# Kernel optimization log

Measured on AMD Instinct MI355X. Metric: run time of the kernel, lower is better.

The kernel has to match this reference:

```python
import jax, jax.numpy as jnp
import numpy as np

SIGMA = 32.0        # Gaussian prior bandwidth (init sigma)
ADJ_RATIO = 0.2     # fraction of neighbors kept per row in feature adjacency
NEG_SLOPE = 0.01    # LeakyReLU slope
EPS = 1e-8


def setup_inputs() -> dict:
    key = jax.random.key(0)
    k0, k1, k2, k3 = jax.random.split(key, 4)
    N, D, L = 8192, 128, 2
    x = jax.random.normal(k0, (N, D), dtype=jnp.float32)
    importances = jax.random.uniform(k1, (N, 1), dtype=jnp.float32)
    W1 = jax.random.normal(k2, (L, D, D), dtype=jnp.float32) / np.float32(np.sqrt(D))
    W2 = jax.random.normal(k3, (L, D, D), dtype=jnp.float32) / np.float32(np.sqrt(D))
    return {"x": x, "importances": importances, "W1": W1, "W2": W2, "batch_size": N}


def _build_adj_prior(imp, eye):
    # Gaussian kernel on pairwise importance differences: [N,N]
    d = imp - imp.T
    A = jnp.exp(-(d * d) / SIGMA) + eye  # self loop
    return A / jnp.sum(A, axis=1, keepdims=True)  # row-normalize


def _build_adj_feature(x, eye, k):
    # cosine similarity, keep top adj_ratio*N entries per row, self loop, row-normalize
    xn = x / (jnp.linalg.norm(x, axis=1, keepdims=True) + EPS)
    S = xn @ xn.T  # [N,N]
    thr = jax.lax.top_k(S, k)[0][:, -1:]  # per-row k-th largest value
    A = jnp.where(S >= thr, S, jnp.zeros_like(S)) + eye
    return A / jnp.sum(A, axis=1, keepdims=True)


def reference(x, importances, W1, W2, batch_size):
    N = batch_size
    k = int(ADJ_RATIO * N)
    eye = jnp.eye(N, dtype=x.dtype)
    L = W1.shape[0]
    h = x
    for l in range(L):  # fixed small layer count
        h = x  # clone before layer (used in final residual)
        adj_prior = _build_adj_prior(importances, eye)
        adj_feat = _build_adj_feature(x, eye, k)
        # graph conv over both adjacencies: A @ (x @ W)
        x = jax.nn.leaky_relu(adj_prior @ (x @ W1[l]) + adj_feat @ (x @ W2[l]),
                              negative_slope=NEG_SLOPE)
    return x + h * importances
```

## Files before the change

kernel.cpp:

```cpp
#include <hip/hip_runtime.h>
#include <hip/hip_bf16.h>

typedef __bf16 bf16x8 __attribute__((ext_vector_type(8)));
typedef float f32x4 __attribute__((ext_vector_type(4)));
typedef unsigned short u16x2 __attribute__((ext_vector_type(2)));
typedef short s16x2 __attribute__((ext_vector_type(2)));
typedef unsigned u32x4 __attribute__((ext_vector_type(4)));
typedef __hip_bfloat16 bf16;

static constexpr int NN = 8192;
static constexpr int DD = 128;
static constexpr int KTOP = 1638;
static constexpr int KSLICE = 8;
static constexpr int KCH = NN / KSLICE;

__device__ __forceinline__ void gll16(const void* g, void* l) {
  __builtin_amdgcn_global_load_lds((const __attribute__((address_space(1))) void*)g,
                                   (__attribute__((address_space(3))) void*)l, 16, 0, 0);
}

__global__ void detect_dtype(const unsigned short* __restrict__ xin, int* __restrict__ flag) {
  __shared__ int cnt;
  if (threadIdx.x == 0) cnt = 0;
  __syncthreads();
  int c = 0;
  for (int i = threadIdx.x; i < 4096; i += 256) {
    int e = (xin[i] >> 7) & 0xFF;
    if (e >= 0x8A) ++c;
  }
  atomicAdd(&cnt, c);
  __syncthreads();
  if (threadIdx.x == 0) *flag = (cnt > 16) ? 1 : 0;
}

__global__ void prep(const void* __restrict__ imp_in,
                     const void* __restrict__ W1, const void* __restrict__ W2,
                     float* __restrict__ impf,
                     bf16* __restrict__ Wt1, bf16* __restrict__ Wt2,
                     const int* __restrict__ flag) {
  int isf32 = *flag;
  int b = blockIdx.x;
  if (b == 0) {
    for (int i = threadIdx.x; i < NN; i += 256)
      impf[i] = isf32 ? ((const float*)imp_in)[i] : __bfloat162float(((const bf16*)imp_in)[i]);
  } else {
    int w = b - 1;
    const void* srcv = (w < 2 ? W1 : W2);
    bf16* dst = (w < 2 ? Wt1 : Wt2) + (w & 1) * DD * DD;
    int off = (w & 1) * DD * DD;
    for (int f = threadIdx.x; f < DD * DD; f += 256) {
      int n = f >> 7, k = f & 127;
      float v = isf32 ? ((const float*)srcv)[off + k * DD + n]
                      : __bfloat162float(((const bf16*)srcv)[off + k * DD + n]);
      dst[n * DD + k] = __float2bfloat16(v);
    }
  }
}

__global__ void rownorm(const void* __restrict__ src, const int* __restrict__ flag, int raw,
                        bf16* __restrict__ xnb, bf16* __restrict__ xb) {
  int wave = threadIdx.x >> 6;
  int lane = threadIdx.x & 63;
  int row = blockIdx.x * 4 + wave;
  float vx, vy;
  if (raw && *flag == 0) {
    unsigned u = ((const unsigned*)src)[(long)row * 64 + lane];
    vx = __uint_as_float(u << 16);
    vy = __uint_as_float(u & 0xFFFF0000u);
  } else {
    float2 v = ((const float2*)src)[(long)row * 64 + lane];
    vx = v.x; vy = v.y;
  }
  float s = vx * vx + vy * vy;
  for (int off = 1; off < 64; off <<= 1) s += __shfl_xor(s, off);
  float inv = 1.0f / (sqrtf(s) + 1e-8f);
  int c = lane * 2;
  xb[(long)row * DD + c]      = __float2bfloat16(vx);
  xb[(long)row * DD + c + 1]  = __float2bfloat16(vy);
  xnb[(long)row * DD + c]     = __float2bfloat16(vx * inv);
  xnb[(long)row * DD + c + 1] = __float2bfloat16(vy * inv);
}

__launch_bounds__(256)
__global__ void prior_reduce(const float* __restrict__ impf, const bf16* __restrict__ Yt1,
                             float* __restrict__ Mt, float* __restrict__ Gt) {
  __shared__ float red[5][4];
  int c = blockIdx.x;
  int tid = threadIdx.x;
  float s[5] = {0.f, 0.f, 0.f, 0.f, 0.f};
  bool hasY = (c < 128);
  const bf16* col = Yt1 + (long)(hasY ? c : 0) * NN;
  for (int j = tid; j < NN; j += 256) {
    float d = impf[j];
    float a = __expf(d * d * (-1.0f / 32.0f));
    float p = hasY ? a * __bfloat162float(col[j]) : a;
    #pragma unroll
    for (int t = 0; t < 5; ++t) { s[t] += p; p *= d; }
  }
  #pragma unroll
  for (int t = 0; t < 5; ++t)
    for (int off = 1; off < 64; off <<= 1) s[t] += __shfl_xor(s[t], off);
  int wave = tid >> 6, lane = tid & 63;
  if (lane == 0)
    #pragma unroll
    for (int t = 0; t < 5; ++t) red[t][wave] = s[t];
  __syncthreads();
  if (tid == 0) {
    #pragma unroll
    for (int t = 0; t < 5; ++t) {
      float v = red[t][0] + red[t][1] + red[t][2] + red[t][3];
      if (hasY) Mt[t * 128 + c] = v; else Gt[t] = v;
    }
  }
}

__device__ __forceinline__ void gemm_core(const bf16* __restrict__ A, const bf16* __restrict__ Bt,
                                          long rowA0, long rowB0, int tid,
                                          bf16* __restrict__ Yt,
                                          bf16* __restrict__ RM, long rm_ld) {
  __shared__ bf16 lA[128][136];
  __shared__ bf16 lB[64][136];
  for (int i = 0; i < 8; ++i) {
    int f = tid + i * 256;
    int r = f >> 4, kg = f & 15;
    *reinterpret_cast<uint4*>(&lA[r][kg * 8]) =
        *reinterpret_cast<const uint4*>(A + (rowA0 + r) * DD + kg * 8);
  }
  for (int i = 0; i < 4; ++i) {
    int f = tid + i * 256;
    int r = f >> 4, kg = f & 15;
    *reinterpret_cast<uint4*>(&lB[r][kg * 8]) =
        *reinterpret_cast<const uint4*>(Bt + (rowB0 + r) * DD + kg * 8);
  }
  __syncthreads();
  int wave = tid >> 6, lane = tid & 63;
  int wm = (wave >> 1) * 64;
  int wn = (wave & 1) * 32;
  int quad = lane >> 4, l16 = lane & 15;
  f32x4 acc[4][2];
  #pragma unroll
  for (int mi = 0; mi < 4; ++mi)
    #pragma unroll
    for (int ni = 0; ni < 2; ++ni) acc[mi][ni] = {0.f, 0.f, 0.f, 0.f};
  #pragma unroll
  for (int ks = 0; ks < 4; ++ks) {
    int kb = ks * 32 + quad * 8;
    bf16x8 af[4], bfr[2];
    #pragma unroll
    for (int mi = 0; mi < 4; ++mi)
      af[mi] = *reinterpret_cast<const bf16x8*>(&lA[wm + mi * 16 + l16][kb]);
    #pragma unroll
    for (int ni = 0; ni < 2; ++ni)
      bfr[ni] = *reinterpret_cast<const bf16x8*>(&lB[wn + ni * 16 + l16][kb]);
    #pragma unroll
    for (int mi = 0; mi < 4; ++mi)
      #pragma unroll
      for (int ni = 0; ni < 2; ++ni)
        acc[mi][ni] = __builtin_amdgcn_mfma_f32_16x16x32_bf16(af[mi], bfr[ni], acc[mi][ni], 0, 0, 0);
  }
  if (Yt) {
    #pragma unroll
    for (int mi = 0; mi < 4; ++mi)
      #pragma unroll
      for (int ni = 0; ni < 2; ++ni) {
        long rowb = rowA0 + wm + mi * 16 + quad * 4;
        long col = rowB0 + wn + ni * 16 + l16;
        bf16 t4[4];
        #pragma unroll
        for (int r = 0; r < 4; ++r) t4[r] = __float2bfloat16(acc[mi][ni][r]);
        *reinterpret_cast<ushort4*>(Yt + col * (long)NN + rowb) =
            *reinterpret_cast<const ushort4*>(t4);
      }
  }
  __syncthreads();
  bf16 (*cs)[72] = reinterpret_cast<bf16(*)[72]>(&lA[0][0]);
  #pragma unroll
  for (int mi = 0; mi < 4; ++mi)
    #pragma unroll
    for (int ni = 0; ni < 2; ++ni)
      #pragma unroll
      for (int r = 0; r < 4; ++r)
        cs[wm + mi * 16 + quad * 4 + r][wn + ni * 16 + l16] = __float2bfloat16(acc[mi][ni][r]);
  __syncthreads();
  #pragma unroll
  for (int i = 0; i < 4; ++i) {
    int f = tid + i * 256;
    int r = f >> 3, sg = f & 7;
    *reinterpret_cast<uint4*>(RM + (rowA0 + r) * rm_ld + rowB0 + sg * 8) =
        *reinterpret_cast<const uint4*>(&cs[r][sg * 8]);
  }
}

__launch_bounds__(256)
__global__ void gemm_s_sym(const bf16* __restrict__ Xn, bf16* __restrict__ S) {
  int bi = blockIdx.y, bj = blockIdx.x;
  if (bj < bi) return;
  __shared__ bf16 lA[128][136];
  __shared__ bf16 lB[128][136];
  int tid = threadIdx.x;
  long rowA0 = (long)bi * 128, rowB0 = (long)bj * 128;
  for (int i = 0; i < 8; ++i) {
    int f = tid + i * 256;
    int r = f >> 4, kg = f & 15;
    *reinterpret_cast<uint4*>(&lA[r][kg * 8]) =
        *reinterpret_cast<const uint4*>(Xn + (rowA0 + r) * DD + kg * 8);
    *reinterpret_cast<uint4*>(&lB[r][kg * 8]) =
        *reinterpret_cast<const uint4*>(Xn + (rowB0 + r) * DD + kg * 8);
  }
  __syncthreads();
  int wave = tid >> 6, lane = tid & 63;
  int wm = (wave >> 1) * 64;
  int wn = (wave & 1) * 64;
  int quad = lane >> 4, l16 = lane & 15;
  f32x4 acc[4][4];
  #pragma unroll
  for (int mi = 0; mi < 4; ++mi)
    #pragma unroll
    for (int ni = 0; ni < 4; ++ni) acc[mi][ni] = {0.f, 0.f, 0.f, 0.f};
  #pragma unroll
  for (int ks = 0; ks < 4; ++ks) {
    int kb = ks * 32 + quad * 8;
    bf16x8 af[4], bfr[4];
    #pragma unroll
    for (int mi = 0; mi < 4; ++mi)
      af[mi] = *reinterpret_cast<const bf16x8*>(&lA[wm + mi * 16 + l16][kb]);
    #pragma unroll
    for (int ni = 0; ni < 4; ++ni)
      bfr[ni] = *reinterpret_cast<const bf16x8*>(&lB[wn + ni * 16 + l16][kb]);
    #pragma unroll
    for (int mi = 0; mi < 4; ++mi)
      #pragma unroll
      for (int ni = 0; ni < 4; ++ni)
        acc[mi][ni] = __builtin_amdgcn_mfma_f32_16x16x32_bf16(af[mi], bfr[ni], acc[mi][ni], 0, 0, 0);
  }
  ushort4 q4[4][4];
  #pragma unroll
  for (int mi = 0; mi < 4; ++mi)
    #pragma unroll
    for (int ni = 0; ni < 4; ++ni) {
      unsigned short t4[4];
      #pragma unroll
      for (int r = 0; r < 4; ++r) {
        float vv = acc[mi][ni][r];
        vv = vv > 0.f ? vv : 0.f;
        bf16 b = __float2bfloat16(vv);
        t4[r] = *reinterpret_cast<unsigned short*>(&b);
      }
      q4[mi][ni] = *reinterpret_cast<const ushort4*>(t4);
    }
  __syncthreads();
  bf16 (*cs)[136]  = reinterpret_cast<bf16(*)[136]>(&lA[0][0]);
  bf16 (*csT)[136] = reinterpret_cast<bf16(*)[136]>(&lB[0][0]);
  #pragma unroll
  for (int mi = 0; mi < 4; ++mi)
    #pragma unroll
    for (int ni = 0; ni < 4; ++ni) {
      int row = wm + mi * 16 + quad * 4;
      int col = wn + ni * 16 + l16;
      const unsigned short* t4 = reinterpret_cast<const unsigned short*>(&q4[mi][ni]);
      #pragma unroll
      for (int r = 0; r < 4; ++r)
        *reinterpret_cast<unsigned short*>(&cs[row + r][col]) = t4[r];
      *reinterpret_cast<ushort4*>(&csT[col][row]) = q4[mi][ni];
    }
  __syncthreads();
  #pragma unroll
  for (int i = 0; i < 8; ++i) {
    int f = tid + i * 256;
    int r = f >> 4, sg = f & 15;
    *reinterpret_cast<uint4*>(S + (rowA0 + r) * NN + rowB0 + sg * 8) =
        *reinterpret_cast<const uint4*>(&cs[r][sg * 8]);
  }
  if (bi != bj) {
    #pragma unroll
    for (int i = 0; i < 8; ++i) {
      int f = tid + i * 256;
      int r = f >> 4, sg = f & 15;
      *reinterpret_cast<uint4*>(S + (rowB0 + r) * NN + rowA0 + sg * 8) =
          *reinterpret_cast<const uint4*>(&csT[r][sg * 8]);
    }
  }
}

__launch_bounds__(256)
__global__ void gemm_y_dual(const bf16* __restrict__ xb,
                            const bf16* __restrict__ Wt1, const bf16* __restrict__ Wt2,
                            bf16* __restrict__ Yt1, bf16* __restrict__ Yt2,
                            bf16* __restrict__ Yr1, bf16* __restrict__ Yr2) {
  int sel = blockIdx.x >> 1;
  int bx = blockIdx.x & 1;
  gemm_core(xb, sel ? Wt2 : Wt1, (long)blockIdx.y * 128, (long)bx * 64, threadIdx.x,
            sel ? Yt2 : Yt1, sel ? Yr2 : Yr1, DD);
}

__launch_bounds__(256)
__global__ void topk_thresh(const bf16* __restrict__ S, unsigned short* __restrict__ kthr,
                            float* __restrict__ invRsF) {
  __shared__ unsigned hist[4][1088];
  int wave = threadIdx.x >> 6, lane = threadIdx.x & 63;
  long row = (long)blockIdx.x * 4 + wave;
  unsigned* h = hist[wave];
  #pragma unroll
  for (int j = 0; j < 17; ++j) h[lane + j * 64] = 0;
  __syncthreads();

  const uint4* rp = reinterpret_cast<const uint4*>(S + row * NN) + lane;
  unsigned hs = 0;
  #pragma unroll
  for (int t = 0; t < 16; ++t) {
    uint4 v = rp[t * 64];
    unsigned a4[4] = {v.x, v.y, v.z, v.w};
    #pragma unroll
    for (int e = 0; e < 4; ++e) {
      unsigned u = a4[e];
      hs |= u;
      s16x2 d = __builtin_bit_cast(s16x2, u) - __builtin_bit_cast(s16x2, 0x3BFF3BFFu);
      d = __builtin_elementwise_max(d, (s16x2)0);
      d = __builtin_elementwise_min(d, (s16x2)1024);
      unsigned bins = __builtin_bit_cast(unsigned, d);
      unsigned blo = bins & 0xFFFFu, bhi = bins >> 16;
      if (blo) atomicAdd(&h[blo], 1u);
      if (bhi) atomicAdd(&h[bhi], 1u);
    }
  }
  __syncthreads();

  unsigned c[17], sfx[17];
  #pragma unroll
  for (int j = 0; j < 17; ++j) c[j] = h[lane * 17 + j];
  unsigned run = 0;
  #pragma unroll
  for (int j = 16; j >= 0; --j) { run += c[j]; sfx[j] = run; }
  unsigned incl = sfx[0];
  #pragma unroll
  for (int off = 1; off < 64; off <<= 1) {
    unsigned t = __shfl_down(incl, off);
    incl += (lane + off < 64) ? t : 0u;
  }
  unsigned above = incl - sfx[0];
  int cand = -1;
  #pragma unroll
  for (int j = 16; j >= 0; --j) {
    int b = lane * 17 + j;
    if (cand < 0 && b >= 1 && above + sfx[j] >= (unsigned)KTOP) cand = b;
  }
  int best = cand;
  #pragma unroll
  for (int off = 1; off < 64; off <<= 1) {
    int t = __shfl_xor(best, off);
    best = t > best ? t : best;
  }
  int thrbin = best >= 1 ? best : 1;
  unsigned thr = 0x3BFFu + (unsigned)thrbin;

  float fs = 0.f;
  #pragma unroll
  for (int j = 0; j < 17; ++j) {
    int b = lane * 17 + j;
    float val = __uint_as_float((0x3BFFu + (unsigned)b) << 16);
    fs += (b >= thrbin) ? (float)c[j] * val : 0.f;
  }
  if (__ballot(hs & 0x40004000u)) {
    float v1024 = __uint_as_float(0x3FFF0000u);
    #pragma unroll 1
    for (int t = 0; t < 16; ++t) {
      uint4 v = rp[t * 64];
      unsigned a4[4] = {v.x, v.y, v.z, v.w};
      for (int e = 0; e < 4; ++e) {
        unsigned lo = a4[e] & 0xFFFFu, hi = a4[e] >> 16;
        if (lo >= 0x4000u && lo < 0x8000u) fs += __uint_as_float(lo << 16) - v1024;
        if (hi >= 0x4000u && hi < 0x8000u) fs += __uint_as_float(hi << 16) - v1024;
      }
    }
  }
  #pragma unroll
  for (int off = 1; off < 64; off <<= 1) fs += __shfl_xor(fs, off);
  if (lane == 0) {
    invRsF[row] = 1.0f / (fs + 1.0f);
    kthr[row] = (unsigned short)thr;
  }
}

__launch_bounds__(256)
__global__ void fused_av_partial(const bf16* __restrict__ S, const bf16* __restrict__ Yt2,
                                 const unsigned short* __restrict__ kthr,
                                 float* __restrict__ Pacc) {
  __shared__ bf16 lS[2][128][64];
  __shared__ bf16 lY[2][128][64];
  int tid = threadIdx.x;
  int wave = tid >> 6, lane = tid & 63;
  long row0 = (long)blockIdx.x * 128;
  long kbase = (long)blockIdx.y * KCH;
  int quad = lane >> 4, l16 = lane & 15;
  int wm = (wave >> 1) * 64;
  int wn = (wave & 1) * 64;
  int swz = (l16 & 7) << 4;

  int sj = lane >> 3, sseg = lane & 7;
  long swb = (long)((sseg ^ sj) << 4);
  const char* gS[4];
  const char* gY[4];
  #pragma unroll
  for (int j = 0; j < 4; ++j) {
    long srow = row0 + (long)(wave * 4 + j) * 8 + sj;
    gS[j] = (const char*)S + (srow * NN + kbase) * 2 + swb;
    long ycol = (long)(wave * 4 + j) * 8 + sj;
    gY[j] = (const char*)Yt2 + (ycol * (long)NN + kbase) * 2 + swb;
  }
  unsigned pp[4];
  #pragma unroll
  for (int mi = 0; mi < 4; ++mi) {
    unsigned p = kthr[row0 + wm + mi * 16 + l16];
    pp[mi] = (p << 16) | p;
  }
  f32x4 acc[4][4];
  #pragma unroll
  for (int mi = 0; mi < 4; ++mi)
    #pragma unroll
    for (int ni = 0; ni < 4; ++ni) acc[mi][ni] = {0.f, 0.f, 0.f, 0.f};

  constexpr int NT = KCH / 64;
  {
    char* lsb = (char*)&lS[0][0][0];
    char* lyb = (char*)&lY[0][0][0];
    #pragma unroll
    for (int j = 0; j < 4; ++j) { gll16(gS[j], lsb + (wave * 4 + j) * 1024); gS[j] += 128; }
    #pragma unroll
    for (int j = 0; j < 4; ++j) { gll16(gY[j], lyb + (wave * 4 + j) * 1024); gY[j] += 128; }
  }
  #pragma unroll 1
  for (int t = 0; t < NT; ++t) {
    int cur = t & 1;
    if (t + 1 < NT) {
      char* lsb = (char*)&lS[cur ^ 1][0][0];
      char* lyb = (char*)&lY[cur ^ 1][0][0];
      #pragma unroll
      for (int j = 0; j < 4; ++j) { gll16(gS[j], lsb + (wave * 4 + j) * 1024); gS[j] += 128; }
      #pragma unroll
      for (int j = 0; j < 4; ++j) { gll16(gY[j], lyb + (wave * 4 + j) * 1024); gY[j] += 128; }
      asm volatile("s_waitcnt vmcnt(8)" ::: "memory");
    } else {
      asm volatile("s_waitcnt vmcnt(0)" ::: "memory");
    }
    __builtin_amdgcn_s_barrier();
    const char* lsb = (const char*)&lS[cur][0][0];
    const char* lyb = (const char*)&lY[cur][0][0];
    #pragma unroll
    for (int ks = 0; ks < 2; ++ks) {
      int cb = ks * 64 + quad * 16;
      int cbs = cb ^ swz;
      bf16x8 av[4], bv[4];
      #pragma unroll
      for (int mi = 0; mi < 4; ++mi) {
        int r = wm + mi * 16 + l16;
        u32x4 uu = *reinterpret_cast<const u32x4*>(lsb + r * 128 + cbs);
        #pragma unroll
        for (int e = 0; e < 4; ++e) {
          unsigned tb = uu[e] | 0x80008000u;
          u16x2 d = __builtin_bit_cast(u16x2, tb) - __builtin_bit_cast(u16x2, pp[mi]);
          s16x2 msk = __builtin_bit_cast(s16x2, d) >> 15;
          uu[e] &= __builtin_bit_cast(unsigned, msk);
        }
        av[mi] = __builtin_bit_cast(bf16x8, uu);
      }
      #pragma unroll
      for (int ni = 0; ni < 4; ++ni) {
        int c = wn + ni * 16 + l16;
        bv[ni] = *reinterpret_cast<const bf16x8*>(lyb + c * 128 + cbs);
      }
      #pragma unroll
      for (int mi = 0; mi < 4; ++mi)
        #pragma unroll
        for (int ni = 0; ni < 4; ++ni)
          acc[mi][ni] = __builtin_amdgcn_mfma_f32_16x16x32_bf16(av[mi], bv[ni], acc[mi][ni], 0, 0, 0);
    }
    __builtin_amdgcn_s_barrier();
  }
  float* out = Pacc + (long)blockIdx.y * NN * DD;
  #pragma unroll
  for (int mi = 0; mi < 4; ++mi)
    #pragma unroll
    for (int ni = 0; ni < 4; ++ni)
      #pragma unroll
      for (int r = 0; r < 4; ++r) {
        long row = row0 + wm + mi * 16 + quad * 4 + r;
        int col = wn + ni * 16 + l16;
        out[row * DD + col] = acc[mi][ni][r];
      }
}

__global__ void epilogue(const float* __restrict__ Pacc, const bf16* __restrict__ Yr1,
                         const bf16* __restrict__ Yr2, const float* __restrict__ Gt,
                         const float* __restrict__ Mt, const float* __restrict__ invRsF,
                         const float* __restrict__ impf,
                         float* __restrict__ Xout, const float* __restrict__ hres,
                         float* __restrict__ outf) {
  int i = blockIdx.x * 256 + threadIdx.x;
  int row = i >> 7, col = i & 127;
  float acc = 0.f;
  #pragma unroll
  for (int s = 0; s < KSLICE; ++s) acc += Pacc[((long)s * NN + row) * DD + col];
  float d = impf[row];
  float a = __expf(d * d * (-1.0f / 32.0f));
  const float ct[5] = {1.0f, 1.0f / 16.0f, 1.0f / 512.0f, 1.0f / 24576.0f, 1.0f / 1572864.0f};
  float g[5];
  float p = a;
  #pragma unroll
  for (int t = 0; t < 5; ++t) { g[t] = ct[t] * p; p *= d; }
  float rs = 1.0f;
  #pragma unroll
  for (int t = 0; t < 5; ++t) rs += g[t] * Gt[t];
  float inv = 1.0f / rs;
  float pv[5];
  #pragma unroll
  for (int t = 0; t < 5; ++t) pv[t] = g[t] * inv;
  float y1 = __bfloat162float(Yr1[i]);
  float y2 = __bfloat162float(Yr2[i]);
  float prior = inv * y1 + pv[0] * Mt[col] + pv[1] * Mt[128 + col] + pv[2] * Mt[256 + col]
              + pv[3] * Mt[384 + col] + pv[4] * Mt[512 + col];
  float v = prior + invRsF[row] * (acc + y2);
  v = v > 0.f ? v : 0.01f * v;
  if (outf) outf[i] = v + hres[i] * impf[row];
  else      Xout[i] = v;
}


extern "C" void kernel_launch(void* const* d_in, const int* in_sizes, int n_in,
                              void* d_out, int out_size, void* d_ws, size_t ws_size,
                              hipStream_t stream) {
  const void* x_in   = d_in[0];
  const void* imp_in = d_in[1];
  const void* W1 = d_in[2];
  const void* W2 = d_in[3];
  float* out = (float*)d_out;

  char* ws = (char*)d_ws;
  size_t o = 0;
  auto alloc = [&](size_t bytes) { void* p = ws + o; o += (bytes + 511) & ~511ull; return p; };
  bf16*  Af   = (bf16*)alloc((size_t)NN * NN * 2);
  float* Pacc = (float*)alloc((size_t)KSLICE * NN * DD * 4);
  float* xf1  = (float*)alloc((size_t)NN * DD * 4);
  bf16*  xnb  = (bf16*)alloc((size_t)NN * DD * 2);
  bf16*  xb   = (bf16*)alloc((size_t)NN * DD * 2);
  bf16*  Yt1  = (bf16*)alloc((size_t)NN * DD * 2);
  bf16*  Yt2  = (bf16*)alloc((size_t)NN * DD * 2);
  bf16*  Yr1  = (bf16*)alloc((size_t)NN * DD * 2);
  bf16*  Yr2  = (bf16*)alloc((size_t)NN * DD * 2);
  bf16*  Wt1  = (bf16*)alloc((size_t)2 * DD * DD * 2);
  bf16*  Wt2  = (bf16*)alloc((size_t)2 * DD * DD * 2);
  float* impf = (float*)alloc((size_t)NN * 4);
  float* Mt   = (float*)alloc((size_t)5 * 128 * 4);
  float* Gt   = (float*)alloc((size_t)8 * 4);
  float* invRsF = (float*)alloc((size_t)NN * 4);
  unsigned short* kthr = (unsigned short*)alloc((size_t)NN * 2);
  int*   dflag  = (int*)alloc(64);
  (void)ws_size; (void)n_in; (void)in_sizes; (void)out_size;

  detect_dtype<<<1, 256, 0, stream>>>((const unsigned short*)x_in, dflag);
  prep<<<5, 256, 0, stream>>>(imp_in, W1, W2, impf, Wt1, Wt2, dflag);

  for (int l = 0; l < 2; ++l) {
    rownorm<<<NN / 4, 256, 0, stream>>>(l ? (const void*)xf1 : x_in, dflag, l ? 0 : 1, xnb, xb);
    gemm_y_dual<<<dim3(4, 64), 256, 0, stream>>>(xb, Wt1 + l * DD * DD, Wt2 + l * DD * DD,
                                                 Yt1, Yt2, Yr1, Yr2);
    prior_reduce<<<129, 256, 0, stream>>>(impf, Yt1, Mt, Gt);
    gemm_s_sym<<<dim3(64, 64), 256, 0, stream>>>(xnb, Af);
    topk_thresh<<<NN / 4, 256, 0, stream>>>(Af, kthr, invRsF);
    fused_av_partial<<<dim3(NN / 128, KSLICE), 256, 0, stream>>>(Af, Yt2, kthr, Pacc);
    if (l == 0)
      epilogue<<<NN * DD / 256, 256, 0, stream>>>(Pacc, Yr1, Yr2, Gt, Mt, invRsF, impf,
                                                  xf1, nullptr, nullptr);
    else
      epilogue<<<NN * DD / 256, 256, 0, stream>>>(Pacc, Yr1, Yr2, Gt, Mt, invRsF, impf,
                                                  nullptr, xf1, out);
  }
}
```

Before: 354.3 us.

## Fuse split-K reduction and epilogue into AV kernel via last-block counter

Folds dtype detection into the prep kernel, removing one launch. It also moves the split-K reduction and epilogue into fused_av_partial: each of the 8 K-slice blocks for a row tile increments an atomic counter, and the last one to finish sums the partials and applies the prior, leaky ReLU and residual with vectorized loads and stores. This drops two epilogue launches and lets the final reduction run while other tiles are still busy. The cost is a threadfence and atomic per block, and the fused tail runs serially on 64 blocks, so it may load-balance poorly.

```diff
diff --git a/kernel.cpp b/kernel.cpp
--- a/kernel.cpp
+++ b/kernel.cpp
@@ -19,28 +19,26 @@
                                    (__attribute__((address_space(3))) void*)l, 16, 0, 0);
 }
 
-__global__ void detect_dtype(const unsigned short* __restrict__ xin, int* __restrict__ flag) {
-  __shared__ int cnt;
-  if (threadIdx.x == 0) cnt = 0;
+__global__ void prep(const unsigned short* __restrict__ xin, const void* __restrict__ imp_in,
+                     const void* __restrict__ W1, const void* __restrict__ W2,
+                     float* __restrict__ impf,
+                     bf16* __restrict__ Wt1, bf16* __restrict__ Wt2,
+                     int* __restrict__ flag, unsigned* __restrict__ avcnt) {
+  __shared__ int cnt_s;
+  if (threadIdx.x == 0) cnt_s = 0;
   __syncthreads();
   int c = 0;
   for (int i = threadIdx.x; i < 4096; i += 256) {
     int e = (xin[i] >> 7) & 0xFF;
     if (e >= 0x8A) ++c;
   }
-  atomicAdd(&cnt, c);
-  __syncthreads();
-  if (threadIdx.x == 0) *flag = (cnt > 16) ? 1 : 0;
-}
-
-__global__ void prep(const void* __restrict__ imp_in,
-                     const void* __restrict__ W1, const void* __restrict__ W2,
-                     float* __restrict__ impf,
-                     bf16* __restrict__ Wt1, bf16* __restrict__ Wt2,
-                     const int* __restrict__ flag) {
-  int isf32 = *flag;
+  atomicAdd(&cnt_s, c);
+  __syncthreads();
+  int isf32 = (cnt_s > 16) ? 1 : 0;
   int b = blockIdx.x;
   if (b == 0) {
+    if (threadIdx.x == 0) *flag = isf32;
+    if (threadIdx.x < 64) avcnt[threadIdx.x] = 0;
     for (int i = threadIdx.x; i < NN; i += 256)
       impf[i] = isf32 ? ((const float*)imp_in)[i] : __bfloat162float(((const bf16*)imp_in)[i]);
   } else {
@@ -384,7 +382,12 @@
 __launch_bounds__(256)
 __global__ void fused_av_partial(const bf16* __restrict__ S, const bf16* __restrict__ Yt2,
                                  const unsigned short* __restrict__ kthr,
-                                 float* __restrict__ Pacc) {
+                                 float* __restrict__ Pacc, unsigned* __restrict__ avcnt,
+                                 const bf16* __restrict__ Yr1, const bf16* __restrict__ Yr2,
+                                 const float* __restrict__ Gt, const float* __restrict__ Mt,
+                                 const float* __restrict__ invRsF, const float* __restrict__ impf,
+                                 float* __restrict__ Xout, const float* __restrict__ hres,
+                                 float* __restrict__ outf) {
   __shared__ bf16 lS[2][128][64];
   __shared__ bf16 lY[2][128][64];
   int tid = threadIdx.x;
@@ -476,7 +479,7 @@
     }
     __builtin_amdgcn_s_barrier();
   }
-  float* out = Pacc + (long)blockIdx.y * NN * DD;
+  float* pout = Pacc + (long)blockIdx.y * NN * DD;
   #pragma unroll
   for (int mi = 0; mi < 4; ++mi)
     #pragma unroll
@@ -485,43 +488,69 @@
       for (int r = 0; r < 4; ++r) {
         long row = row0 + wm + mi * 16 + quad * 4 + r;
         int col = wn + ni * 16 + l16;
-        out[row * DD + col] = acc[mi][ni][r];
+        pout[row * DD + col] = acc[mi][ni][r];
       }
-}
-
-__global__ void epilogue(const float* __restrict__ Pacc, const bf16* __restrict__ Yr1,
-                         const bf16* __restrict__ Yr2, const float* __restrict__ Gt,
-                         const float* __restrict__ Mt, const float* __restrict__ invRsF,
-                         const float* __restrict__ impf,
-                         float* __restrict__ Xout, const float* __restrict__ hres,
-                         float* __restrict__ outf) {
-  int i = blockIdx.x * 256 + threadIdx.x;
-  int row = i >> 7, col = i & 127;
-  float acc = 0.f;
-  #pragma unroll
-  for (int s = 0; s < KSLICE; ++s) acc += Pacc[((long)s * NN + row) * DD + col];
-  float d = impf[row];
-  float a = __expf(d * d * (-1.0f / 32.0f));
-  const float ct[5] = {1.0f, 1.0f / 16.0f, 1.0f / 512.0f, 1.0f / 24576.0f, 1.0f / 1572864.0f};
-  float g[5];
-  float p = a;
-  #pragma unroll
-  for (int t = 0; t < 5; ++t) { g[t] = ct[t] * p; p *= d; }
-  float rs = 1.0f;
-  #pragma unroll
-  for (int t = 0; t < 5; ++t) rs += g[t] * Gt[t];
-  float inv = 1.0f / rs;
-  float pv[5];
-  #pragma unroll
-  for (int t = 0; t < 5; ++t) pv[t] = g[t] * inv;
-  float y1 = __bfloat162float(Yr1[i]);
-  float y2 = __bfloat162float(Yr2[i]);
-  float prior = inv * y1 + pv[0] * Mt[col] + pv[1] * Mt[128 + col] + pv[2] * Mt[256 + col]
-              + pv[3] * Mt[384 + col] + pv[4] * Mt[512 + col];
-  float v = prior + invRsF[row] * (acc + y2);
-  v = v > 0.f ? v : 0.01f * v;
-  if (outf) outf[i] = v + hres[i] * impf[row];
-  else      Xout[i] = v;
+
+  __threadfence();
+  __shared__ int lastF;
+  if (tid == 0) {
+    unsigned old = atomicAdd(&avcnt[blockIdx.x], 1u);
+    lastF = (old == (unsigned)(KSLICE - 1));
+  }
+  __syncthreads();
+  if (!lastF) return;
+  __threadfence();
+  if (tid == 0) avcnt[blockIdx.x] = 0;
+  #pragma unroll 1
+  for (int it = 0; it < 16; ++it) {
+    int q = tid + it * 256;
+    int r = q >> 5, c4 = (q & 31) << 2;
+    long row = row0 + r;
+    long i = row * DD + c4;
+    f32x4 a4 = {0.f, 0.f, 0.f, 0.f};
+    #pragma unroll
+    for (int s = 0; s < KSLICE; ++s)
+      a4 += *reinterpret_cast<const f32x4*>(&Pacc[((long)s * NN + row) * DD + c4]);
+    float d = impf[row];
+    float a = __expf(d * d * (-1.0f / 32.0f));
+    const float ct[5] = {1.0f, 1.0f / 16.0f, 1.0f / 512.0f, 1.0f / 24576.0f, 1.0f / 1572864.0f};
+    float g[5];
+    float p = a;
+    #pragma unroll
+    for (int t = 0; t < 5; ++t) { g[t] = ct[t] * p; p *= d; }
+    float rs = 1.0f;
+    #pragma unroll
+    for (int t = 0; t < 5; ++t) rs += g[t] * Gt[t];
+    float inv = 1.0f / rs;
+    float pvv[5];
+    #pragma unroll
+    for (int t = 0; t < 5; ++t) pvv[t] = g[t] * inv;
+    float ir = invRsF[row];
+    ushort4 y1u = *reinterpret_cast<const ushort4*>(Yr1 + i);
+    ushort4 y2u = *reinterpret_cast<const ushort4*>(Yr2 + i);
+    const bf16* y1p = reinterpret_cast<const bf16*>(&y1u);
+    const bf16* y2p = reinterpret_cast<const bf16*>(&y2u);
+    f32x4 res;
+    #pragma unroll
+    for (int k = 0; k < 4; ++k) {
+      float y1 = __bfloat162float(y1p[k]);
+      float y2 = __bfloat162float(y2p[k]);
+      int col = c4 + k;
+      float prior = inv * y1 + pvv[0] * Mt[col] + pvv[1] * Mt[128 + col]
+                  + pvv[2] * Mt[256 + col] + pvv[3] * Mt[384 + col] + pvv[4] * Mt[512 + col];
+      float v = prior + ir * (a4[k] + y2);
+      v = v > 0.f ? v : 0.01f * v;
+      res[k] = v;
+    }
+    if (outf) {
+      f32x4 h4 = *reinterpret_cast<const f32x4*>(&hres[i]);
+      #pragma unroll
+      for (int k = 0; k < 4; ++k) res[k] = res[k] + h4[k] * d;
+      *reinterpret_cast<f32x4*>(&outf[i]) = res;
+    } else {
+      *reinterpret_cast<f32x4*>(&Xout[i]) = res;
+    }
+  }
 }
 
 
@@ -554,10 +583,11 @@
   float* invRsF = (float*)alloc((size_t)NN * 4);
   unsigned short* kthr = (unsigned short*)alloc((size_t)NN * 2);
   int*   dflag  = (int*)alloc(64);
+  unsigned* avcnt = (unsigned*)alloc(64 * 4);
   (void)ws_size; (void)n_in; (void)in_sizes; (void)out_size;
 
-  detect_dtype<<<1, 256, 0, stream>>>((const unsigned short*)x_in, dflag);
-  prep<<<5, 256, 0, stream>>>(imp_in, W1, W2, impf, Wt1, Wt2, dflag);
+  prep<<<5, 256, 0, stream>>>((const unsigned short*)x_in, imp_in, W1, W2,
+                              impf, Wt1, Wt2, dflag, avcnt);
 
   for (int l = 0; l < 2; ++l) {
     rownorm<<<NN / 4, 256, 0, stream>>>(l ? (const void*)xf1 : x_in, dflag, l ? 0 : 1, xnb, xb);
@@ -566,12 +596,13 @@
     prior_reduce<<<129, 256, 0, stream>>>(impf, Yt1, Mt, Gt);
     gemm_s_sym<<<dim3(64, 64), 256, 0, stream>>>(xnb, Af);
     topk_thresh<<<NN / 4, 256, 0, stream>>>(Af, kthr, invRsF);
-    fused_av_partial<<<dim3(NN / 128, KSLICE), 256, 0, stream>>>(Af, Yt2, kthr, Pacc);
     if (l == 0)
-      epilogue<<<NN * DD / 256, 256, 0, stream>>>(Pacc, Yr1, Yr2, Gt, Mt, invRsF, impf,
-                                                  xf1, nullptr, nullptr);
+      fused_av_partial<<<dim3(NN / 128, KSLICE), 256, 0, stream>>>(
+          Af, Yt2, kthr, Pacc, avcnt, Yr1, Yr2, Gt, Mt, invRsF, impf,
+          xf1, nullptr, nullptr);
     else
-      epilogue<<<NN * DD / 256, 256, 0, stream>>>(Pacc, Yr1, Yr2, Gt, Mt, invRsF, impf,
-                                                  nullptr, xf1, out);
-  }
-}
+      fused_av_partial<<<dim3(NN / 128, KSLICE), 256, 0, stream>>>(
+          Af, Yt2, kthr, Pacc, avcnt, Yr1, Yr2, Gt, Mt, invRsF, impf,
+          nullptr, xf1, out);
+  }
+}
```

Result: slower. 506.3 us (+42.9%).
